# Optimization experiments

Hardware: AMD Instinct MI355X
Metric: run time of the kernel (lower is better)

The kernel has to match this reference:

```python
import jax, jax.numpy as jnp
import numpy as np

EPS = 1e-5

def mean_variance_norm(x):
    # x: [b, c, h, w]; per-(b,c) instance norm over spatial, unbiased var (torch default)
    b, c, h, w = x.shape
    xf = x.reshape(b, c, h * w)
    mean = xf.mean(axis=2)
    var = xf.var(axis=2, ddof=1) + EPS
    std = jnp.sqrt(var)
    return (x - mean[:, :, None, None]) / std[:, :, None, None]

def conv1x1(x, w, b):
    # w: [out_c, in_c], b: [out_c]
    return jnp.einsum('oc,bchw->bohw', w, x) + b[None, :, None, None]

def setup_inputs() -> dict:
    key = jax.random.key(0)
    ks = jax.random.split(key, 10)
    b, C, H, W = 4, 512, 64, 64
    content = jax.random.normal(ks[0], (b, C, H, W), dtype=jnp.float32)
    style = jax.random.normal(ks[1], (b, C, H, W), dtype=jnp.float32)
    def w_(k, o, i):
        return jax.random.normal(k, (o, i), dtype=jnp.float32) * 0.02
    def b_(k, o):
        return jax.random.normal(k, (o,), dtype=jnp.float32) * 0.02
    return {
        'content': content, 'style': style,
        'f_w': w_(ks[2], C, C), 'f_b': b_(ks[3], C),
        'g_w': w_(ks[4], C, C), 'g_b': b_(ks[5], C),
        'h_w': w_(ks[6], C, C), 'h_b': b_(ks[7], C),
        'out_w': w_(ks[8], C, C), 'out_b': b_(ks[9], C),
    }

def reference(content, style, f_w, f_b, g_w, g_b, h_w, h_b, out_w, out_b):
    b, C, h, w = content.shape
    F = conv1x1(mean_variance_norm(content), f_w, f_b)   # [b,C,h,w]
    G = conv1x1(mean_variance_norm(style), g_w, g_b)     # [b,C,hg,wg]
    H = conv1x1(style, h_w, h_b)                          # [b,C,hg,wg]
    # spatial <= max_sample, so no subsampling branch
    Gf = G.reshape(b, C, -1)                              # [b,C,M]
    Hf = H.reshape(b, C, -1)                              # [b,C,M]
    Ff = F.reshape(b, C, -1)                              # [b,C,N]
    S = jnp.einsum('bcn,bcm->bnm', Ff, Gf)                # [b,N,M]
    S = jax.nn.softmax(S, axis=-1)
    styled = jnp.einsum('bcm,bnm->bcn', Hf, S)            # [b,C,N]
    styled = styled.reshape(b, C, h, w)
    return conv1x1(styled, out_w, out_b)
```

## Files before the change

### kernel.cpp

```cpp
#include <hip/hip_runtime.h>
#include <hip/hip_bf16.h>

typedef _Float16 f16;
typedef __attribute__((ext_vector_type(8))) _Float16 half8;
typedef __attribute__((ext_vector_type(4))) _Float16 half4;
typedef __attribute__((ext_vector_type(4))) float f32x4;

#define AS1 __attribute__((address_space(1)))
#define AS3 __attribute__((address_space(3)))

constexpr int CH  = 512;
constexpr int NSP = 4096;
constexpr int NB  = 4;

#define VM8  asm volatile("s_waitcnt vmcnt(8)"  ::: "memory")
#define VM0  asm volatile("s_waitcnt vmcnt(0)"  ::: "memory")
#define BARS do { __builtin_amdgcn_s_barrier(); asm volatile("" ::: "memory"); } while (0)

__device__ __forceinline__ void gload_lds16(const void* g, void* l) {
    __builtin_amdgcn_global_load_lds((const AS1 void*)g, (AS3 void*)l, 16, 0, 0);
}

__global__ void transpose_f16_kernel(const float* __restrict__ content, const float* __restrict__ style,
                                     f16* __restrict__ content_t, f16* __restrict__ style_t,
                                     float* __restrict__ raw)
{
    int b = blockIdx.z & 3, is_style = blockIdx.z >> 2;
    const float* src = (is_style ? style : content) + (size_t)b * CH * NSP;
    f16* dst = (is_style ? style_t : content_t) + (size_t)b * NSP * CH;
    int c0 = blockIdx.y * 64, n0 = blockIdx.x * 64;
    __shared__ f16 tile[64][72];
    int t = threadIdx.x;
    #pragma unroll
    for (int i = 0; i < 4; i++) {
        int idx = t + i*256;
        int cr = idx >> 4, n4 = (idx & 15) * 4;
        float4 v = *(const float4*)(src + (size_t)(c0+cr)*NSP + n0 + n4);
        tile[cr][n4+0] = (f16)v.x; tile[cr][n4+1] = (f16)v.y;
        tile[cr][n4+2] = (f16)v.z; tile[cr][n4+3] = (f16)v.w;
    }
    __syncthreads();
    {
        int row = t >> 2, seg = (t & 3) * 16;
        float s1 = 0.f, s2 = 0.f;
        #pragma unroll
        for (int j = 0; j < 16; j++) {
            float x = (float)tile[row][seg + j];
            s1 += x; s2 += x * x;
        }
        s1 += __shfl_down(s1, 2, 4); s1 += __shfl_down(s1, 1, 4);
        s2 += __shfl_down(s2, 2, 4); s2 += __shfl_down(s2, 1, 4);
        if ((t & 3) == 0) {
            int si = is_style * 2 * NB * CH + b * CH + c0 + row;
            atomicAdd(&raw[si], s1);
            atomicAdd(&raw[si + NB * CH], s2);
        }
    }
    int nr = t >> 2, seg = (t & 3) * 16;
    __align__(16) f16 out_v[16];
    #pragma unroll
    for (int j = 0; j < 16; j++) out_v[j] = tile[seg + j][nr];
    f16* dp = dst + (size_t)(n0+nr)*CH + c0 + seg;
    *(int4*)dp = ((int4*)out_v)[0];
    *(int4*)(dp + 8) = ((int4*)out_v)[1];
}

__global__ void effw_kernel(const float* __restrict__ fw, const float* __restrict__ fb,
                            const float* __restrict__ gw, const float* __restrict__ gb,
                            const float* __restrict__ hw, const float* __restrict__ ow,
                            const float* __restrict__ raw,
                            f16* __restrict__ fw_e, float* __restrict__ fb_e,
                            f16* __restrict__ gw_e, float* __restrict__ gb_e,
                            f16* __restrict__ hw_h, f16* __restrict__ ow_h)
{
    int o = blockIdx.x, b = blockIdx.y, mode = blockIdx.z, t = threadIdx.x;
    if (mode >= 2) {
        if (b != 0) return;
        const float* srcw = (mode == 2) ? hw : ow;
        f16* dstw = (mode == 2) ? hw_h : ow_h;
        for (int c = t; c < CH; c += 128) dstw[o*CH + c] = (f16)srcw[o*CH + c];
        return;
    }
    const float* w  = mode ? gw : fw;
    const float* rw = raw + (mode ? 2*NB*CH : 0);
    f16* we = mode ? gw_e : fw_e;
    float part = 0.f;
    for (int c = t; c < CH; c += 128) {
        float s1 = rw[b*CH + c], s2 = rw[NB*CH + b*CH + c];
        float mn = s1 * (1.f/NSP);
        float var = (s2 - (float)NSP*mn*mn) * (1.f/(NSP-1));
        float is = rsqrtf(var + 1e-5f);
        float wv = w[o*CH + c];
        we[((size_t)b*CH + o)*CH + c] = (f16)(wv * is);
        part += wv * mn * is;
    }
    #pragma unroll
    for (int off = 32; off; off >>= 1) part += __shfl_down(part, off);
    __shared__ float rr[2];
    if ((t & 63) == 0) rr[t >> 6] = part;
    __syncthreads();
    if (t == 0) (mode ? gb_e : fb_e)[b*CH + o] = (mode ? gb : fb)[o] - (rr[0] + rr[1]);
}

__global__ __launch_bounds__(256)
void conv3_kernel(const f16* __restrict__ fw_e, const float* __restrict__ fb_e,
                  const f16* __restrict__ gw_e, const float* __restrict__ gb_e,
                  const f16* __restrict__ hw_h, const float* __restrict__ h_b,
                  const f16* __restrict__ content_t, const f16* __restrict__ style_t,
                  f16* __restrict__ F_t, f16* __restrict__ G_t, f16* __restrict__ H_)
{
    const int T = gridDim.x;
    const int bid = blockIdx.x;
    const int tile = (bid & 7) * (T >> 3) + (bid >> 3);
    const int zz = tile >> 7, rem = tile & 127;
    const int mt = rem >> 5, nt = rem & 31;
    const int kind = zz >> 2, b = zz & 3;

    const f16* W; const float* bias; const f16* Xt; f16* Y;
    if (kind == 0)      { W = fw_e + (size_t)b*CH*CH; bias = fb_e + b*CH; Xt = content_t + (size_t)b*NSP*CH; Y = F_t + (size_t)b*NSP*CH; }
    else if (kind == 1) { W = gw_e + (size_t)b*CH*CH; bias = gb_e + b*CH; Xt = style_t + (size_t)b*NSP*CH; Y = G_t + (size_t)b*NSP*CH; }
    else                { W = hw_h;                    bias = h_b;         Xt = style_t + (size_t)b*NSP*CH; Y = H_ + (size_t)b*CH*NSP; }

    const int m0 = mt * 128, n0 = nt * 128;
    const int t = threadIdx.x, wave = t >> 6, lane = t & 63;
    const int l15 = lane & 15, l4 = lane >> 4;
    const int wm = (wave >> 1) * 64, wn = (wave & 1) * 64;

    __shared__ __align__(16) f16 Al[8192];
    __shared__ __align__(16) f16 Bl[8192];

    f32x4 acc[4][4] = {};

    for (int ks = 0; ks < CH/64; ks++) {
        const int kk = ks * 64;
        #pragma unroll
        for (int j = 0; j < 4; j++) {
            int L  = ((wave*4 + j)*64 + lane) * 16;
            int SL = L ^ (((L >> 7) & 7) << 4);
            int row = SL >> 7, seg = (SL & 127) >> 1;
            gload_lds16(W  + (size_t)(m0 + row)*CH + kk + seg, &Al[L >> 1]);
            gload_lds16(Xt + (size_t)(n0 + row)*CH + kk + seg, &Bl[L >> 1]);
        }
        VM0; BARS;
        #pragma unroll
        for (int kb = 0; kb < 2; kb++) {
            half8 a[4], bb[4];
            #pragma unroll
            for (int i = 0; i < 4; i++) {
                int ab = (wm + i*16 + l15)*128 + kb*64 + l4*16;
                ab ^= ((ab >> 7) & 7) << 4;
                a[i] = *(const half8*)&Al[ab >> 1];
                int bby = (wn + i*16 + l15)*128 + kb*64 + l4*16;
                bby ^= ((bby >> 7) & 7) << 4;
                bb[i] = *(const half8*)&Bl[bby >> 1];
            }
            #pragma unroll
            for (int i = 0; i < 4; i++)
                #pragma unroll
                for (int jj = 0; jj < 4; jj++)
                    acc[i][jj] = __builtin_amdgcn_mfma_f32_16x16x32_f16(a[i], bb[jj], acc[i][jj], 0, 0, 0);
        }
        BARS;
    }

    #pragma unroll
    for (int i = 0; i < 4; i++) {
        const int ob = m0 + wm + i*16 + l4*4;
        f32x4 bv = *(const f32x4*)(bias + ob);
        #pragma unroll
        for (int jj = 0; jj < 4; jj++) {
            const int n = n0 + wn + jj*16 + l15;
            f32x4 v = acc[i][jj];
            v[0] += bv[0]; v[1] += bv[1]; v[2] += bv[2]; v[3] += bv[3];
            if (kind < 2) {
                half4 pk; pk[0]=(f16)v[0]; pk[1]=(f16)v[1]; pk[2]=(f16)v[2]; pk[3]=(f16)v[3];
                *(half4*)(Y + (size_t)n * CH + ob) = pk;
            } else {
                #pragma unroll
                for (int r = 0; r < 4; r++) Y[(size_t)(ob + r) * NSP + n] = (f16)v[r];
            }
        }
    }
}

template<int MODE>
__global__ __launch_bounds__(256)
void gemm_kernel(const f16* __restrict__ W, long wstrideb,
                 const f16* __restrict__ Xt, long xstrideb,
                 const float* __restrict__ bias, long bstrideb,
                 void* __restrict__ Y, long ystrideb,
                 int K, long ostride)
{
    const int z = blockIdx.z;
    W    += (size_t)z * wstrideb;
    Xt   += (size_t)z * xstrideb;
    bias += (size_t)z * bstrideb;
    const int m0 = blockIdx.y * 128, n0 = blockIdx.x * 128;
    const int t = threadIdx.x, wave = t >> 6, lane = t & 63;
    const int l15 = lane & 15, l4 = lane >> 4;
    const int wm = (wave >> 1) * 64, wn = (wave & 1) * 64;

    __shared__ __align__(16) f16 Al[2][8192];
    __shared__ __align__(16) f16 Bl[2][8192];

    f32x4 acc[4][4] = {};

    auto stage = [&](int bufi, int kk) {
        #pragma unroll
        for (int j = 0; j < 4; j++) {
            int L  = ((wave*4 + j)*64 + lane) * 16;
            int SL = L ^ (((L >> 7) & 7) << 4);
            int row = SL >> 7, seg = (SL & 127) >> 1;
            gload_lds16(W  + (size_t)(m0 + row)*K + kk + seg, &Al[bufi][L >> 1]);
            gload_lds16(Xt + (size_t)(n0 + row)*K + kk + seg, &Bl[bufi][L >> 1]);
        }
    };

    const int nks = K >> 6;
    stage(0, 0);
    for (int ks = 0; ks < nks; ks++) {
        int bufi = ks & 1;
        if (ks < nks-1) { stage(bufi ^ 1, (ks + 1) * 64); VM8; }
        else            { VM0; }
        BARS;
        #pragma unroll
        for (int kb = 0; kb < 2; kb++) {
            half8 a[4], bb[4];
            #pragma unroll
            for (int i = 0; i < 4; i++) {
                int ab = (wm + i*16 + l15)*128 + kb*64 + l4*16;
                ab ^= ((ab >> 7) & 7) << 4;
                a[i] = *(const half8*)&Al[bufi][ab >> 1];
                int bby = (wn + i*16 + l15)*128 + kb*64 + l4*16;
                bby ^= ((bby >> 7) & 7) << 4;
                bb[i] = *(const half8*)&Bl[bufi][bby >> 1];
            }
            #pragma unroll
            for (int i = 0; i < 4; i++)
                #pragma unroll
                for (int jj = 0; jj < 4; jj++)
                    acc[i][jj] = __builtin_amdgcn_mfma_f32_16x16x32_f16(a[i], bb[jj], acc[i][jj], 0, 0, 0);
        }
        BARS;
    }

    #pragma unroll
    for (int i = 0; i < 4; i++) {
        const int ob = m0 + wm + i*16 + l4*4;
        f32x4 bv = *(const f32x4*)(bias + ob);
        #pragma unroll
        for (int jj = 0; jj < 4; jj++) {
            const int n = n0 + wn + jj*16 + l15;
            f32x4 v = acc[i][jj];
            v[0] += bv[0]; v[1] += bv[1]; v[2] += bv[2]; v[3] += bv[3];
            float* Yf = (float*)Y + (size_t)z * ystrideb;
            #pragma unroll
            for (int r = 0; r < 4; r++) Yf[(size_t)(ob + r) * ostride + n] = v[r];
        }
    }
}

template<int TPB, int NCT>
__global__ __launch_bounds__(256)
void gemm_att_kernel(const f16* __restrict__ W, long wstrideb,
                     const f16* __restrict__ Xt, long xstrideb,
                     f16* __restrict__ Y, long ystrideb,
                     int K, long ostride)
{
    const int T = gridDim.x;
    const int bid = blockIdx.x;
    const int tile = (bid & 7) * (T >> 3) + (bid >> 3);
    const int z = tile / TPB, rem = tile - z * TPB;
    const int mt = rem / NCT, nt = rem - mt * NCT;
    W  += (size_t)z * wstrideb;
    Xt += (size_t)z * xstrideb;
    f16* Yb = Y + (size_t)z * ystrideb;
    const int m0 = mt * 128, n0 = nt * 128;

    const int t = threadIdx.x, wave = t >> 6, lane = t & 63;
    const int l15 = lane & 15, l4 = lane >> 4;
    const int wm = (wave >> 1) * 64, wn = (wave & 1) * 64;

    __shared__ __align__(16) f16 Al[8192];
    __shared__ __align__(16) f16 Bl[8192];

    f32x4 acc[4][4] = {};

    const int nks = K >> 6;
    for (int ks = 0; ks < nks; ks++) {
        const int kk = ks * 64;
        #pragma unroll
        for (int j = 0; j < 4; j++) {
            int L  = ((wave*4 + j)*64 + lane) * 16;
            int SL = L ^ (((L >> 7) & 7) << 4);
            int row = SL >> 7, seg = (SL & 127) >> 1;
            gload_lds16(W  + (size_t)(m0 + row)*K + kk + seg, &Al[L >> 1]);
            gload_lds16(Xt + (size_t)(n0 + row)*K + kk + seg, &Bl[L >> 1]);
        }
        VM0; BARS;
        #pragma unroll
        for (int kb = 0; kb < 2; kb++) {
            half8 a[4], bb[4];
            #pragma unroll
            for (int i = 0; i < 4; i++) {
                int ab = (wm + i*16 + l15)*128 + kb*64 + l4*16;
                ab ^= ((ab >> 7) & 7) << 4;
                a[i] = *(const half8*)&Al[ab >> 1];
                int bby = (wn + i*16 + l15)*128 + kb*64 + l4*16;
                bby ^= ((bby >> 7) & 7) << 4;
                bb[i] = *(const half8*)&Bl[bby >> 1];
            }
            #pragma unroll
            for (int i = 0; i < 4; i++)
                #pragma unroll
                for (int jj = 0; jj < 4; jj++)
                    acc[i][jj] = __builtin_amdgcn_mfma_f32_16x16x32_f16(a[i], bb[jj], acc[i][jj], 0, 0, 0);
        }
        BARS;
    }

    #pragma unroll
    for (int i = 0; i < 4; i++) {
        const int ob = m0 + wm + i*16 + l4*4;
        #pragma unroll
        for (int jj = 0; jj < 4; jj++) {
            const int ncol = n0 + wn + jj*16 + l15;
            #pragma unroll
            for (int r = 0; r < 4; r++)
                Yb[(size_t)(ob + r) * ostride + ncol] = (f16)acc[i][jj][r];
        }
    }
}

template<int NCT>
__global__ __launch_bounds__(256)
void pv_split_kernel(const f16* __restrict__ S, long sstride,
                     const f16* __restrict__ Hm, long hstride,
                     f16* __restrict__ P0, f16* __restrict__ P1,
                     long pstride, int Khalf)
{
    const int T = gridDim.x;
    const int bid = blockIdx.x;
    const int tile = (bid & 7) * (T >> 3) + (bid >> 3);
    const int TPB = 32 * NCT;
    const int sp = tile / (NB * TPB);
    int rem = tile - sp * NB * TPB;
    const int z = rem / TPB; rem -= z * TPB;
    const int mt = rem / NCT, nt = rem - mt * NCT;
    const f16* W  = S  + (size_t)z * sstride + (size_t)sp * Khalf;
    const f16* Xt = Hm + (size_t)z * hstride + (size_t)sp * Khalf;
    f16* Yb = (sp ? P1 : P0) + (size_t)z * pstride;
    const int m0 = mt * 128, n0 = nt * 128;

    const int t = threadIdx.x, wave = t >> 6, lane = t & 63;
    const int l15 = lane & 15, l4 = lane >> 4;
    const int wm = (wave >> 1) * 64, wn = (wave & 1) * 64;

    __shared__ __align__(16) f16 Al[8192];
    __shared__ __align__(16) f16 Bl[8192];

    f32x4 acc[4][4] = {};

    const int nks = Khalf >> 6;
    for (int ks = 0; ks < nks; ks++) {
        const int kk = ks * 64;
        #pragma unroll
        for (int j = 0; j < 4; j++) {
            int L  = ((wave*4 + j)*64 + lane) * 16;
            int SL = L ^ (((L >> 7) & 7) << 4);
            int row = SL >> 7, seg = (SL & 127) >> 1;
            gload_lds16(W  + (size_t)(m0 + row)*NSP + kk + seg, &Al[L >> 1]);
            gload_lds16(Xt + (size_t)(n0 + row)*NSP + kk + seg, &Bl[L >> 1]);
        }
        VM0; BARS;
        #pragma unroll
        for (int kb = 0; kb < 2; kb++) {
            half8 a[4], bb[4];
            #pragma unroll
            for (int i = 0; i < 4; i++) {
                int ab = (wm + i*16 + l15)*128 + kb*64 + l4*16;
                ab ^= ((ab >> 7) & 7) << 4;
                a[i] = *(const half8*)&Al[ab >> 1];
                int bby = (wn + i*16 + l15)*128 + kb*64 + l4*16;
                bby ^= ((bby >> 7) & 7) << 4;
                bb[i] = *(const half8*)&Bl[bby >> 1];
            }
            #pragma unroll
            for (int i = 0; i < 4; i++)
                #pragma unroll
                for (int jj = 0; jj < 4; jj++)
                    acc[i][jj] = __builtin_amdgcn_mfma_f32_16x16x32_f16(a[i], bb[jj], acc[i][jj], 0, 0, 0);
        }
        BARS;
    }

    #pragma unroll
    for (int i = 0; i < 4; i++) {
        const int ob = m0 + wm + i*16 + l4*4;
        #pragma unroll
        for (int jj = 0; jj < 4; jj++) {
            const int ncol = n0 + wn + jj*16 + l15;
            #pragma unroll
            for (int r = 0; r < 4; r++)
                Yb[(size_t)(ob + r) * CH + ncol] = (f16)acc[i][jj][r];
        }
    }
}

__global__ __launch_bounds__(256)
void reduce_pv_kernel(const f16* __restrict__ p0, const f16* __restrict__ p1, f16* __restrict__ out)
{
    size_t i = ((size_t)blockIdx.x * 256 + threadIdx.x) * 8;
    half8 a = *(const half8*)(p0 + i);
    half8 b = *(const half8*)(p1 + i);
    half8 o;
    #pragma unroll
    for (int e = 0; e < 8; e++) o[e] = (f16)((float)a[e] + (float)b[e]);
    *(half8*)(out + i) = o;
}

__global__ __launch_bounds__(256)
void softmax_kernel(f16* __restrict__ S, int nrows)
{
    int row = blockIdx.x * 4 + (threadIdx.x >> 6);
    if (row >= nrows) return;
    int lane = threadIdx.x & 63;
    f16* p = S + (size_t)row * NSP + lane * 8;

    half8 v[8];
    #pragma unroll
    for (int j = 0; j < 8; j++) v[j] = *(const half8*)(p + j * 512);

    float mx = -1e30f;
    #pragma unroll
    for (int j = 0; j < 8; j++)
        #pragma unroll
        for (int e = 0; e < 8; e++) mx = fmaxf(mx, (float)v[j][e]);
    #pragma unroll
    for (int off = 32; off; off >>= 1) mx = fmaxf(mx, __shfl_xor(mx, off));

    float ex[64];
    float s = 0.f;
    #pragma unroll
    for (int j = 0; j < 8; j++)
        #pragma unroll
        for (int e = 0; e < 8; e++) {
            float x = __expf((float)v[j][e] - mx);
            ex[j*8 + e] = x; s += x;
        }
    #pragma unroll
    for (int off = 32; off; off >>= 1) s += __shfl_xor(s, off);
    float inv = 1.0f / s;

    #pragma unroll
    for (int j = 0; j < 8; j++) {
        half8 o;
        #pragma unroll
        for (int e = 0; e < 8; e++) o[e] = (f16)(ex[j*8 + e] * inv);
        *(half8*)(p + j * 512) = o;
    }
}

extern "C" void kernel_launch(void* const* d_in, const int* in_sizes, int n_in,
                              void* d_out, int out_size, void* d_ws, size_t ws_size,
                              hipStream_t stream)
{
    const float* content = (const float*)d_in[0];
    const float* style   = (const float*)d_in[1];
    const float* f_w = (const float*)d_in[2];
    const float* f_b = (const float*)d_in[3];
    const float* g_w = (const float*)d_in[4];
    const float* g_b = (const float*)d_in[5];
    const float* h_w = (const float*)d_in[6];
    const float* h_b = (const float*)d_in[7];
    const float* o_w = (const float*)d_in[8];
    const float* o_b = (const float*)d_in[9];

    char* ws = (char*)d_ws;
    size_t off = 0;
    auto alloc = [&](size_t bytes) -> void* {
        void* p = ws + off;
        off += (bytes + 255) & ~(size_t)255;
        return p;
    };
    float* raw = (float*)alloc(4 * NB*CH * 4);
    f16* fw_e = (f16*)alloc((size_t)NB*CH*CH*2);
    f16* gw_e = (f16*)alloc((size_t)NB*CH*CH*2);
    f16* hw_h = (f16*)alloc((size_t)CH*CH*2);
    f16* ow_h = (f16*)alloc((size_t)CH*CH*2);
    float* fb_e = (float*)alloc((size_t)NB*CH*4);
    float* gb_e = (float*)alloc((size_t)NB*CH*4);
    f16* content_t = (f16*)alloc((size_t)NB*NSP*CH*2);
    f16* style_t   = (f16*)alloc((size_t)NB*NSP*CH*2);
    f16* F_t = (f16*)alloc((size_t)NB*NSP*CH*2);
    f16* G_t = (f16*)alloc((size_t)NB*NSP*CH*2);
    f16* H_  = (f16*)alloc((size_t)NB*CH*NSP*2);
    f16* styled_t = content_t;

    size_t s_plane = (size_t)NSP * NSP;
    bool all4 = (off + 4 * s_plane * 2 <= ws_size);
    f16* S16 = (f16*)alloc((all4 ? 4 : 1) * s_plane * 2);
    if (off > ws_size) return;

    hipMemsetAsync(raw, 0, 4 * NB*CH * 4, stream);
    transpose_f16_kernel<<<dim3(NSP/64, CH/64, NB*2), dim3(256), 0, stream>>>(
        content, style, content_t, style_t, raw);
    effw_kernel<<<dim3(CH, NB, 4), dim3(128), 0, stream>>>(f_w, f_b, g_w, g_b, h_w, o_w, raw,
                                                           fw_e, fb_e, gw_e, gb_e, hw_h, ow_h);
    conv3_kernel<<<dim3(12*128), dim3(256), 0, stream>>>(
        fw_e, fb_e, gw_e, gb_e, hw_h, h_b, content_t, style_t, F_t, G_t, H_);

    if (all4) {
        gemm_att_kernel<1024,32><<<dim3(NB*1024), dim3(256), 0, stream>>>(
            F_t, (long)NSP*CH, G_t, (long)NSP*CH, S16, (long)s_plane, CH, (long)NSP);
        softmax_kernel<<<dim3(NB*NSP/4), dim3(256), 0, stream>>>(S16, NB*NSP);
        pv_split_kernel<4><<<dim3(1024), dim3(256), 0, stream>>>(
            S16, (long)s_plane, H_, (long)CH*NSP, F_t, G_t, (long)NSP*CH, NSP/2);
        reduce_pv_kernel<<<dim3((int)((size_t)NB*NSP*CH/2048)), dim3(256), 0, stream>>>(F_t, G_t, styled_t);
    } else {
        for (int b = 0; b < NB; b++) {
            gemm_att_kernel<1024,32><<<dim3(1024), dim3(256), 0, stream>>>(
                F_t + (size_t)b*NSP*CH, 0L, G_t + (size_t)b*NSP*CH, 0L,
                S16, 0L, CH, (long)NSP);
            softmax_kernel<<<dim3(NSP/4), dim3(256), 0, stream>>>(S16, NSP);
            gemm_att_kernel<128,4><<<dim3(128), dim3(256), 0, stream>>>(
                S16, 0L, H_ + (size_t)b*CH*NSP, 0L,
                styled_t + (size_t)b*NSP*CH, 0L, NSP, (long)CH);
        }
    }

    gemm_kernel<2><<<dim3(NSP/128, CH/128, NB), dim3(256), 0, stream>>>(
        ow_h, 0L, styled_t, (long)NSP*CH, o_b, 0L, d_out, (long)CH*NSP, CH, (long)NSP);
}
```

Before: 311.4 us.

## Replace attention GEMMs with 256x256-tile double-buffered pipelined kernel

```diff
diff --git a/kernel.cpp b/kernel.cpp
--- a/kernel.cpp
+++ b/kernel.cpp
@@ -14,8 +14,13 @@
 constexpr int NB  = 4;
 
 #define VM8  asm volatile("s_waitcnt vmcnt(8)"  ::: "memory")
+#define VM6  asm volatile("s_waitcnt vmcnt(6)"  ::: "memory")
+#define VM4  asm volatile("s_waitcnt vmcnt(4)"  ::: "memory")
+#define VM2  asm volatile("s_waitcnt vmcnt(2)"  ::: "memory")
 #define VM0  asm volatile("s_waitcnt vmcnt(0)"  ::: "memory")
 #define BARS do { __builtin_amdgcn_s_barrier(); asm volatile("" ::: "memory"); } while (0)
+#define SP1  __builtin_amdgcn_s_setprio(1)
+#define SP0  __builtin_amdgcn_s_setprio(0)
 
 __device__ __forceinline__ void gload_lds16(const void* g, void* l) {
     __builtin_amdgcn_global_load_lds((const AS1 void*)g, (AS3 void*)l, 16, 0, 0);
@@ -332,77 +337,142 @@
     }
 }
 
-template<int NCT>
-__global__ __launch_bounds__(256)
-void pv_split_kernel(const f16* __restrict__ S, long sstride,
-                     const f16* __restrict__ Hm, long hstride,
-                     f16* __restrict__ P0, f16* __restrict__ P1,
-                     long pstride, int Khalf)
+template<int TPB, int NCT, int SPLITK>
+__global__ __launch_bounds__(512)
+void gemm256_kernel(const f16* __restrict__ W, long wstrideb,
+                    const f16* __restrict__ Xt, long xstrideb,
+                    f16* __restrict__ Y0, f16* __restrict__ Y1, long ystrideb,
+                    int K, int kstride, long ostride)
 {
     const int T = gridDim.x;
     const int bid = blockIdx.x;
     const int tile = (bid & 7) * (T >> 3) + (bid >> 3);
-    const int TPB = 32 * NCT;
-    const int sp = tile / (NB * TPB);
-    int rem = tile - sp * NB * TPB;
+    int rem = tile, sp = 0;
+    if constexpr (SPLITK == 2) { sp = tile / (NB * TPB); rem = tile - sp * NB * TPB; }
     const int z = rem / TPB; rem -= z * TPB;
     const int mt = rem / NCT, nt = rem - mt * NCT;
-    const f16* W  = S  + (size_t)z * sstride + (size_t)sp * Khalf;
-    const f16* Xt = Hm + (size_t)z * hstride + (size_t)sp * Khalf;
-    f16* Yb = (sp ? P1 : P0) + (size_t)z * pstride;
-    const int m0 = mt * 128, n0 = nt * 128;
-
-    const int t = threadIdx.x, wave = t >> 6, lane = t & 63;
+    const f16* Wb = W  + (size_t)z * wstrideb + (size_t)sp * K;
+    const f16* Xb = Xt + (size_t)z * xstrideb + (size_t)sp * K;
+    f16* Yb = ((SPLITK == 2 && sp) ? Y1 : Y0) + (size_t)z * ystrideb;
+    const int m0 = mt * 256, n0 = nt * 256;
+
+    const int t = threadIdx.x, lane = t & 63, wave = t >> 6;
     const int l15 = lane & 15, l4 = lane >> 4;
-    const int wm = (wave >> 1) * 64, wn = (wave & 1) * 64;
-
-    __shared__ __align__(16) f16 Al[8192];
-    __shared__ __align__(16) f16 Bl[8192];
-
-    f32x4 acc[4][4] = {};
-
-    const int nks = Khalf >> 6;
-    for (int ks = 0; ks < nks; ks++) {
-        const int kk = ks * 64;
+    const int wr = wave >> 2, wc = wave & 3;
+
+    __shared__ __align__(16) f16 As[2][16384];
+    __shared__ __align__(16) f16 Bs[2][16384];
+
+    f32x4 acc[8][4] = {};
+
+    auto stA = [&](int nbuf, int kk, int half, int q) {
+        int L  = half*16384 + q*8192 + t*16;
+        int SL = L ^ (((L >> 7) & 7) << 4);
+        gload_lds16(Wb + (size_t)(m0 + (SL >> 7)) * kstride + kk + ((SL & 127) >> 1), &As[nbuf][L >> 1]);
+    };
+    auto stB = [&](int nbuf, int kk, int half, int q) {
+        int L  = half*16384 + q*8192 + t*16;
+        int SL = L ^ (((L >> 7) & 7) << 4);
+        gload_lds16(Xb + (size_t)(n0 + (SL >> 7)) * kstride + kk + ((SL & 127) >> 1), &Bs[nbuf][L >> 1]);
+    };
+    auto ldA = [&](int buf, int i, int kb) {
+        int L = (((i&3)*16) + wr*64 + ((i>>2)*128) + l15)*128 + kb*64 + l4*16;
+        L ^= ((L >> 7) & 7) << 4;
+        return *(const half8*)&As[buf][L >> 1];
+    };
+    auto ldB = [&](int buf, int j, int kb) {
+        int L = (((j&1)*16) + wc*32 + ((j>>1)*128) + l15)*128 + kb*64 + l4*16;
+        L ^= ((L >> 7) & 7) << 4;
+        return *(const half8*)&Bs[buf][L >> 1];
+    };
+
+    const int nks = K >> 6;
+    stA(0,0,0,0); stA(0,0,0,1);
+    stB(0,0,0,0); stB(0,0,0,1);
+    stB(0,0,1,0); stB(0,0,1,1);
+    stA(0,0,1,0); stA(0,0,1,1);
+    VM4;
+    if (nks > 1) {
+        stA(1,64,0,0); stA(1,64,0,1);
+        stB(1,64,0,0); stB(1,64,0,1);
+        stB(1,64,1,0); stB(1,64,1,1);
+        VM6;
+    } else { VM0; }
+    BARS;
+
+    half8 a[4][2], b01[2][2], b23[2][2];
+
+    for (int kt = 0; kt < nks; kt++) {
+        const int buf = kt & 1;
+        const int kk1 = (kt+1) << 6, kk2 = (kt+2) << 6;
+        const bool s1 = (kt+1 < nks), s2 = (kt+2 < nks);
+
+        #pragma unroll
+        for (int i = 0; i < 4; i++) { a[i][0] = ldA(buf, i, 0); a[i][1] = ldA(buf, i, 1); }
+        #pragma unroll
+        for (int j = 0; j < 2; j++) { b01[j][0] = ldB(buf, j, 0); b01[j][1] = ldB(buf, j, 1); }
+        if (s1) { stA(buf^1, kk1, 1, 0); stA(buf^1, kk1, 1, 1); }
+        else    { VM2; }
+        BARS; SP1;
+        #pragma unroll
+        for (int i = 0; i < 4; i++)
+            #pragma unroll
+            for (int j = 0; j < 2; j++)
+                #pragma unroll
+                for (int kb = 0; kb < 2; kb++)
+                    acc[i][j] = __builtin_amdgcn_mfma_f32_16x16x32_f16(a[i][kb], b01[j][kb], acc[i][j], 0, 0, 0);
+        SP0; BARS;
+
+        #pragma unroll
+        for (int j = 0; j < 2; j++) { b23[j][0] = ldB(buf, 2+j, 0); b23[j][1] = ldB(buf, 2+j, 1); }
+        if (s2)       { stA(buf, kk2, 0, 0); stA(buf, kk2, 0, 1); }
+        else if (!s1) { VM0; }
+        BARS; SP1;
+        #pragma unroll
+        for (int i = 0; i < 4; i++)
+            #pragma unroll
+            for (int j = 0; j < 2; j++)
+                #pragma unroll
+                for (int kb = 0; kb < 2; kb++)
+                    acc[i][2+j] = __builtin_amdgcn_mfma_f32_16x16x32_f16(a[i][kb], b23[j][kb], acc[i][2+j], 0, 0, 0);
+        SP0; BARS;
+
+        #pragma unroll
+        for (int i = 0; i < 4; i++) { a[i][0] = ldA(buf, 4+i, 0); a[i][1] = ldA(buf, 4+i, 1); }
+        if (s2) { stB(buf, kk2, 0, 0); stB(buf, kk2, 0, 1); }
+        BARS; SP1;
+        #pragma unroll
+        for (int i = 0; i < 4; i++)
+            #pragma unroll
+            for (int j = 0; j < 2; j++)
+                #pragma unroll
+                for (int kb = 0; kb < 2; kb++)
+                    acc[4+i][2+j] = __builtin_amdgcn_mfma_f32_16x16x32_f16(a[i][kb], b23[j][kb], acc[4+i][2+j], 0, 0, 0);
+        SP0; BARS;
+
+        if (s2)      { stB(buf, kk2, 1, 0); stB(buf, kk2, 1, 1); VM6; }
+        else if (s1) { VM4; }
+        BARS; SP1;
+        #pragma unroll
+        for (int i = 0; i < 4; i++)
+            #pragma unroll
+            for (int j = 0; j < 2; j++)
+                #pragma unroll
+                for (int kb = 0; kb < 2; kb++)
+                    acc[4+i][j] = __builtin_amdgcn_mfma_f32_16x16x32_f16(a[i][kb], b01[j][kb], acc[4+i][j], 0, 0, 0);
+        SP0; BARS;
+    }
+
+    #pragma unroll
+    for (int i = 0; i < 8; i++) {
+        const int ob = m0 + ((i&3)*16) + wr*64 + ((i>>2)*128) + l4*4;
         #pragma unroll
         for (int j = 0; j < 4; j++) {
-            int L  = ((wave*4 + j)*64 + lane) * 16;
-            int SL = L ^ (((L >> 7) & 7) << 4);
-            int row = SL >> 7, seg = (SL & 127) >> 1;
-            gload_lds16(W  + (size_t)(m0 + row)*NSP + kk + seg, &Al[L >> 1]);
-            gload_lds16(Xt + (size_t)(n0 + row)*NSP + kk + seg, &Bl[L >> 1]);
-        }
-        VM0; BARS;
-        #pragma unroll
-        for (int kb = 0; kb < 2; kb++) {
-            half8 a[4], bb[4];
-            #pragma unroll
-            for (int i = 0; i < 4; i++) {
-                int ab = (wm + i*16 + l15)*128 + kb*64 + l4*16;
-                ab ^= ((ab >> 7) & 7) << 4;
-                a[i] = *(const half8*)&Al[ab >> 1];
-                int bby = (wn + i*16 + l15)*128 + kb*64 + l4*16;
-                bby ^= ((bby >> 7) & 7) << 4;
-                bb[i] = *(const half8*)&Bl[bby >> 1];
-            }
-            #pragma unroll
-            for (int i = 0; i < 4; i++)
-                #pragma unroll
-                for (int jj = 0; jj < 4; jj++)
-                    acc[i][jj] = __builtin_amdgcn_mfma_f32_16x16x32_f16(a[i], bb[jj], acc[i][jj], 0, 0, 0);
-        }
-        BARS;
-    }
-
-    #pragma unroll
-    for (int i = 0; i < 4; i++) {
-        const int ob = m0 + wm + i*16 + l4*4;
-        #pragma unroll
-        for (int jj = 0; jj < 4; jj++) {
-            const int ncol = n0 + wn + jj*16 + l15;
+            const int ncol = n0 + ((j&1)*16) + wc*32 + ((j>>1)*128) + l15;
+            f32x4 v = acc[i][j];
             #pragma unroll
             for (int r = 0; r < 4; r++)
-                Yb[(size_t)(ob + r) * CH + ncol] = (f16)acc[i][jj][r];
+                Yb[(size_t)(ob + r) * ostride + ncol] = (f16)v[r];
         }
     }
 }
@@ -511,11 +581,11 @@
         fw_e, fb_e, gw_e, gb_e, hw_h, h_b, content_t, style_t, F_t, G_t, H_);
 
     if (all4) {
-        gemm_att_kernel<1024,32><<<dim3(NB*1024), dim3(256), 0, stream>>>(
-            F_t, (long)NSP*CH, G_t, (long)NSP*CH, S16, (long)s_plane, CH, (long)NSP);
+        gemm256_kernel<256,16,1><<<dim3(1024), dim3(512), 0, stream>>>(
+            F_t, (long)NSP*CH, G_t, (long)NSP*CH, S16, nullptr, (long)s_plane, CH, CH, (long)NSP);
         softmax_kernel<<<dim3(NB*NSP/4), dim3(256), 0, stream>>>(S16, NB*NSP);
-        pv_split_kernel<4><<<dim3(1024), dim3(256), 0, stream>>>(
-            S16, (long)s_plane, H_, (long)CH*NSP, F_t, G_t, (long)NSP*CH, NSP/2);
+        gemm256_kernel<32,2,2><<<dim3(256), dim3(512), 0, stream>>>(
+            S16, (long)s_plane, H_, (long)CH*NSP, F_t, G_t, (long)NSP*CH, NSP/2, NSP, (long)CH);
         reduce_pv_kernel<<<dim3((int)((size_t)NB*NSP*CH/2048)), dim3(256), 0, stream>>>(F_t, G_t, styled_t);
     } else {
         for (int b = 0; b < NB; b++) {
```

Result: faster. 291.6 us (-6.4%).
